# Kernel optimization log

Measured on AMD Instinct MI355X. Metric: run time of the kernel, lower is better.

## Reference

```python
import math
import jax, jax.numpy as jnp
import numpy as np

# ---- hard-coded constants from the source module ----
T_H = 1.5; M = 60; DT = T_H / M; SQDT = math.sqrt(DT)
ALPHA = 0.8; RHO = 0.3; SQ1MR2 = math.sqrt(1.0 - RHO * RHO)
GAMMA = 5.0; KAPPA_Y = 1.2; LB_W = 1e-3
R = 0.02; SIGMA = 0.2; SIGMA_Y = 0.3; THETA_Y = 0.0; PI_CAP = 2.0
RPTS = 128       # sub_batch (one accumulation iteration)
REPEATS = 128    # total repeats == sub_batch -> single loop pass
N_PTS = 32       # number of eval states
HID = 64


def setup_inputs():
    key = jax.random.key(0)
    ks = jax.random.split(key, 8)
    W = 0.8 + 0.4 * jax.random.uniform(ks[0], (N_PTS, 1), jnp.float32)   # W0_range
    Y = -1.0 + 2.0 * jax.random.uniform(ks[1], (N_PTS, 1), jnp.float32)  # Y0_range
    TmT = jnp.full((N_PTS, 1), T_H, jnp.float32)
    B = RPTS * N_PTS
    # [sim(+/-), draw(z1/z2), step, path, 1] -- fresh noise per antithetic branch, as in torch
    noise = jax.random.normal(ks[2], (2, 2, M, B, 1), jnp.float32)
    w1 = 0.1 * jax.random.normal(ks[3], (3, HID), jnp.float32)
    b1 = jnp.zeros((HID,), jnp.float32)
    w2 = 0.1 * jax.random.normal(ks[4], (HID, HID), jnp.float32)
    b2 = jnp.zeros((HID,), jnp.float32)
    w3 = 0.1 * jax.random.normal(ks[5], (HID, 1), jnp.float32)
    b3 = jnp.zeros((1,), jnp.float32)
    return {"W": W, "TmT": TmT, "Y": Y, "noise": noise,
            "w1": w1, "b1": b1, "w2": w2, "b2": b2, "w3": w3, "b3": b3}


def _policy(params, W, TmT, Y):
    w1, b1, w2, b2, w3, b3 = params
    x = jnp.concatenate([W, TmT, Y], axis=-1)          # [B,3]
    h = jnp.tanh(x @ w1 + b1)
    h = jnp.tanh(h @ w2 + b2)
    return h @ w3 + b3                                 # [B,1]


def _simulate(params, W0, Y0, z1, z2, anti):
    """60-step Euler-Maruyama; returns CRRA utility U(W_T), shape [B,1]."""
    logW = jnp.log(jnp.clip(W0, LB_W, None))
    TmT0 = jnp.full_like(W0, T_H)

    def step(carry, zs):
        logW, Y, TmT = carry
        z1s, z2s = zs
        pi = _policy(params, jnp.exp(logW), TmT, Y)
        zW = anti * z1s
        zY = anti * (RHO * z1s + SQ1MR2 * z2s)
        drift = R + pi * (SIGMA * ALPHA * Y)
        var = (pi * SIGMA) ** 2
        logW = logW + (drift - 0.5 * var) * DT + pi * SIGMA * SQDT * zW
        Y = Y + KAPPA_Y * (THETA_Y - Y) * DT + SIGMA_Y * SQDT * zY
        logW = jnp.log(jnp.clip(jnp.exp(logW), LB_W, None))
        return (logW, Y, TmT - DT), None

    (logW, _, _), _ = jax.lax.scan(step, (logW, Y0, TmT0), (z1, z2))
    W_T = jnp.exp(logW)
    return W_T ** (1.0 - GAMMA) / (1.0 - GAMMA)        # gamma != 1


def reference(W, TmT, Y, noise, w1, b1, w2, b2, w3, b3):
    params = (w1, b1, w2, b2, w3, b3)
    n = W.shape[0]
    Wd = jax.lax.stop_gradient(W)   # forward detaches W, Y
    Yd = jax.lax.stop_gradient(Y)
    W0 = jnp.tile(Wd, (RPTS, 1))    # [B,1]
    Y0 = jnp.tile(Yd, (RPTS, 1))
    z1p, z2p = noise[0, 0], noise[0, 1]
    z1m, z2m = noise[1, 0], noise[1, 1]

    def f(W0_, Y0_):
        U = 0.5 * (_simulate(params, W0_, Y0_, z1p, z2p, 1.0)
                   + _simulate(params, W0_, Y0_, z1m, z2m, -1.0))
        # U_avg.sum() as in torch: mean over rpts, sum over eval points
        return jnp.sum(jnp.mean(U.reshape(RPTS, n), axis=0))

    lam_full = jax.grad(f, 0)(W0, Y0)                  # [B,1]

    def g(W0_, Y0_):
        # lam.view(rpts,n,1).mean(0).sum() == sum(lam_full)/rpts
        return jnp.sum(jax.grad(f, 0)(W0_, Y0_)) / RPTS

    dW_full, dY_full = jax.grad(g, (0, 1))(W0, Y0)     # [B,1] each

    inv = 1.0 / REPEATS   # faithful to source accumulation scaling
    lam = lam_full.reshape(RPTS, n, 1).mean(0) * inv
    dlamW = dW_full.reshape(RPTS, n, 1).mean(0) * inv
    dlamY = dY_full.reshape(RPTS, n, 1).mean(0) * inv

    # project_pmp
    mu_minus_r = SIGMA * (ALPHA * Yd)
    coeff = -1.0 / (Wd * dlamW + 1e-8)
    myo = coeff * (lam * (mu_minus_r / SIGMA ** 2))
    hedge = coeff * (SIGMA * RHO * SIGMA_Y * dlamY / SIGMA ** 2)
    return jnp.clip(myo + hedge, -PI_CAP, PI_CAP)      # [n,1]
```

## Files before the change

kernel.cpp:

```cpp
#include <hip/hip_runtime.h>
#include <math.h>

#define HID    64
#define MSTEPS 60
#define NPTS   32
#define RPTSC  128
#define BTOT   (RPTSC*NPTS)
#define NSIM   (2*BTOT)
#define NWAVE  (NSIM/2)
#define NBLK   (NWAVE/4)

#define C_DT     0.025f
#define C_SQDT   0.15811388300841897f
#define C_ALPHA  0.8f
#define C_RHO    0.3f
#define C_SQ1MR2 0.9539392014169456f
#define C_KAPPA  1.2f
#define C_R      0.02f
#define C_SIGMA  0.2f
#define C_SIGY   0.3f
#define C_LBW    1e-3f
#define C_LOGLBW -6.907755279f
#define C_2L2E   2.8853900817779268f

#define WAVE_LDS 3584
#define OFF_DV   2304
#define OFF_DA   3328

typedef _Float16 half8 __attribute__((ext_vector_type(8)));
typedef float    f32x4 __attribute__((ext_vector_type(4)));
typedef _Float16 h2    __attribute__((ext_vector_type(2)));
typedef int      i32x2 __attribute__((ext_vector_type(2)));
typedef int      i32x4 __attribute__((ext_vector_type(4)));

__device__ __forceinline__ float rlanef(float v, int l) {
    return __int_as_float(__builtin_amdgcn_readlane(__float_as_int(v), l));
}
template <int OFF>
__device__ __forceinline__ float swz(float v) {
    return __int_as_float(__builtin_amdgcn_ds_swizzle(__float_as_int(v), OFF));
}
__device__ __forceinline__ f32x4 MFMA(half8 a, half8 b, f32x4 c) {
    return __builtin_amdgcn_mfma_f32_16x16x32_f16(a, b, c, 0, 0, 0);
}
__device__ __forceinline__ int pk16(float a, float b) {
    return __builtin_bit_cast(int, __builtin_amdgcn_cvt_pkrtz(a, b));
}
__device__ __forceinline__ h2 pk2(float a, float b) {
    return __builtin_bit_cast(h2, __builtin_amdgcn_cvt_pkrtz(a, b));
}
__device__ __forceinline__ unsigned permu(unsigned s0, unsigned s1, unsigned sel) {
    return __builtin_amdgcn_perm(s0, s1, sel);
}
__device__ __forceinline__ h2 permh(unsigned s0, unsigned s1, unsigned sel) {
    return __builtin_bit_cast(h2, __builtin_amdgcn_perm(s0, s1, sel));
}
__device__ __forceinline__ float tanh_fast(float xs) {
    return 1.0f - 2.0f * __builtin_amdgcn_rcpf(__builtin_amdgcn_exp2f(xs) + 1.0f);
}
__device__ __forceinline__ i32x2 tr16(unsigned a) {
    i32x2 d;
    asm volatile("ds_read_b64_tr_b16 %0, %1"
                 : "=&v"(d) : "v"(a) : "memory");
    return d;
}
#define LGKM0_FENCE() do { \
    asm volatile("s_waitcnt lgkmcnt(0)" ::: "memory"); \
    __builtin_amdgcn_sched_barrier(0); } while (0)

__global__ __launch_bounds__(256, 4) void sim_kernel(
    const float* __restrict__ noise,
    const float* __restrict__ w1, const float* __restrict__ b1,
    const float* __restrict__ w2, const float* __restrict__ b2,
    const float* __restrict__ w3, const float* __restrict__ b3,
    const float* __restrict__ Wp, const float* __restrict__ Yp,
    float* __restrict__ sd)
{
    __shared__ __align__(16) char smem[4 * WAVE_LDS];
    const int lane = threadIdx.x & 63;
    const int quad = lane >> 4;
    const int mrow = lane & 15;
    const int par  = lane >> 5;
    char* wb = smem + (threadIdx.x >> 6) * WAVE_LDS;

    const int w = __builtin_amdgcn_readfirstlane(
        (int)((blockIdx.x * blockDim.x + threadIdx.x) >> 6));
    const int simb = w >> 11;
    const int pg   = 2*(w & 2047) + par;
    const int i    = pg & (NPTS - 1);

    const float cW  = w1[lane];
    const float cT  = w1[HID + lane];
    const float cYw = w1[2*HID + lane];
    const float b1k = b1[lane];
    const float b2k = b2[lane];
    const float b3v = b3[0];
    const float cW_s  = cW  * C_2L2E;
    const float cT_s  = cT  * C_2L2E;
    const float cYw_s = cYw * C_2L2E;
    const float b1_s  = b1k * C_2L2E;
    const float b2_s  = b2k * C_2L2E;
    const h2 cWh  = pk2(cW, cW);
    const h2 cYwh = pk2(cYw, cYw);
    const h2 cW2m = pk2(-2.0f*cW*cW,  -2.0f*cW*cW);
    const h2 cWYm = pk2(-2.0f*cW*cYw, -2.0f*cW*cYw);
    const h2 hone = {(_Float16)1.0f,  (_Float16)1.0f};
    const h2 m2h  = {(_Float16)-2.0f, (_Float16)-2.0f};

    half8 B00, B01, B02, B03, B10, B11, B12, B13, W30, W31;
    {
        half8 h;
        #define LOADB(dst, q, t) \
            { for (int j = 0; j < 8; ++j) \
                h[j] = (_Float16)w2[((q)*32 + quad*8 + j)*HID + (t)*16 + mrow]; \
              dst = h; }
        LOADB(B00, 0, 0) LOADB(B01, 0, 1) LOADB(B02, 0, 2) LOADB(B03, 0, 3)
        LOADB(B10, 1, 0) LOADB(B11, 1, 1) LOADB(B12, 1, 2) LOADB(B13, 1, 3)
        #undef LOADB
        for (int j = 0; j < 8; ++j) h[j] = (_Float16)w3[0*32 + quad*8 + j];
        W30 = h;
        for (int j = 0; j < 8; ++j) h[j] = (_Float16)w3[1*32 + quad*8 + j];
        W31 = h;
    }
    asm volatile("" : "+v"(B00), "+v"(B01), "+v"(B02), "+v"(B03),
                      "+v"(B10), "+v"(B11), "+v"(B12), "+v"(B13),
                      "+v"(W30), "+v"(W31));

    char* Swp = wb + (lane >> 2) * 144 + (lane & 3) * 32;
    const unsigned wbu  = (unsigned)(size_t)wb;
    const unsigned tA0 = wbu + quad*288 + mrow*2;
    const unsigned tA1 = tA0 + 144;
    const unsigned tB0 = tA0 + 1152;
    const unsigned tB1 = tA0 + 1296;

    const float* zp1 = noise + (size_t)(simb*2 + 0) * MSTEPS * BTOT + pg;
    const float* zp2 = noise + (size_t)(simb*2 + 1) * MSTEPS * BTOT + pg;

    const float anti = simb ? -1.0f : 1.0f;
    const float ksa  = C_SIGMA * C_ALPHA;
    const float ks2  = C_SIGMA * C_SIGMA;
    const float ksn  = anti * C_SIGMA * C_SQDT;
    const float kFy  = ksa * C_DT;
    const float ksd  = ks2 * C_DT;
    const float kv   = 0.5f * ks2 * C_DT;
    const float kRdt = C_R * C_DT;
    const float ky1  = anti * C_SIGY * C_SQDT * C_RHO;
    const float ky2  = anti * C_SIGY * C_SQDT * C_SQ1MR2;
    const float cYfac = 1.0f - C_KAPPA * C_DT;

    const float W0 = Wp[i];
    float L   = __logf(fmaxf(W0, C_LBW));
    float W   = __expf(L);
    float Yv  = Yp[i];
    float tmt = 1.5f;
    float gW  = 1.0f / W0;
    float hWW = -gW * gW;
    float gY  = 0.0f, hWY = 0.0f;
    float cYt = 1.0f;

    #pragma unroll 1
    for (int m = 0; m < MSTEPS; ++m) {
        const float z1 = zp1[(size_t)m * BTOT];
        const float z2 = zp2[(size_t)m * BTOT];

        const float Wb0 = rlanef(W, 0),  Wb1 = rlanef(W, 32);
        const float Yb0 = rlanef(Yv, 0), Yb1 = rlanef(Yv, 32);

        const float base1s = fmaf(tmt, cT_s, b1_s);
        {
            const float t10 = tanh_fast(fmaf(Wb0, cW_s, fmaf(Yb0, cYw_s, base1s)));
            const float t11 = tanh_fast(fmaf(Wb1, cW_s, fmaf(Yb1, cYw_s, base1s)));
            const h2 tp  = pk2(t10, t11);
            const h2 dpp = hone - tp * tp;
            const h2 ddq = tp * dpp;
            const h2 r1 = dpp * cWh;
            const h2 r2 = dpp * cYwh;
            const h2 r3 = ddq * cW2m;
            const h2 r4 = ddq * cWYm;
            const unsigned utp = __builtin_bit_cast(unsigned, tp);
            const unsigned ur1 = __builtin_bit_cast(unsigned, r1);
            const unsigned ur2 = __builtin_bit_cast(unsigned, r2);
            const unsigned ur3 = __builtin_bit_cast(unsigned, r3);
            const unsigned ur4 = __builtin_bit_cast(unsigned, r4);
            i32x4 lo, hi;
            lo[0] = (int)permu(ur1, utp, 0x05040100u);
            lo[1] = (int)permu(ur3, ur2, 0x05040100u);
            lo[2] = (int)(ur4 & 0xFFFFu);
            lo[3] = 0;
            hi[0] = (int)permu(ur1, utp, 0x07060302u);
            hi[1] = (int)permu(ur3, ur2, 0x07060302u);
            hi[2] = (int)(ur4 >> 16);
            hi[3] = 0;
            *(i32x4*)(Swp)      = lo;
            *(i32x4*)(Swp + 16) = hi;
        }

        i32x2 ta0 = tr16(tA0), ta1 = tr16(tA1);
        i32x2 tb0 = tr16(tB0), tb1 = tr16(tB1);
        LGKM0_FENCE();
        i32x4 ia0; ia0[0]=ta0[0]; ia0[1]=ta0[1]; ia0[2]=ta1[0]; ia0[3]=ta1[1];
        i32x4 ia1; ia1[0]=tb0[0]; ia1[1]=tb0[1]; ia1[2]=tb1[0]; ia1[3]=tb1[1];
        half8 af0 = __builtin_bit_cast(half8, ia0);
        half8 af1 = __builtin_bit_cast(half8, ia1);

        f32x4 acc[4];
        const f32x4 zz = {0.f, 0.f, 0.f, 0.f};
        acc[0] = MFMA(af1, B10, MFMA(af0, B00, zz));
        acc[1] = MFMA(af1, B11, MFMA(af0, B01, zz));
        acc[2] = MFMA(af1, B12, MFMA(af0, B02, zz));
        acc[3] = MFMA(af1, B13, MFMA(af0, B03, zz));

        {
            const int p = quad >> 1;
            if (!(quad & 1)) {
                #pragma unroll
                for (int t = 0; t < 4; ++t) {
                    int2 v;
                    v.x = pk16(acc[t].x, acc[t].y);
                    v.y = pk16(acc[t].z, acc[t].w);
                    *(int2*)(wb + OFF_DV + ((t*16 + mrow) << 4) + (p << 3)) = v;
                }
            } else {
                #pragma unroll
                for (int t = 0; t < 4; ++t)
                    *(_Float16*)(wb + OFF_DA + ((t*16 + mrow) << 2) + (p << 1)) =
                        (_Float16)acc[t].x;
            }
        }

        const f32x4 dvv = *(const f32x4*)(wb + OFF_DV + lane*16);
        const h2 awyp   = *(const h2*)(wb + OFF_DA + lane*4);
        {
            const unsigned q0 = __builtin_bit_cast(unsigned, dvv.x);
            const unsigned q1 = __builtin_bit_cast(unsigned, dvv.y);
            const unsigned q2 = __builtin_bit_cast(unsigned, dvv.z);
            const unsigned q3 = __builtin_bit_cast(unsigned, dvv.w);
            const h2 a0p  = permh(q2, q0, 0x05040100);
            const h2 aWp  = permh(q2, q0, 0x07060302);
            const h2 aYp  = permh(q3, q1, 0x05040100);
            const h2 aWWp = permh(q3, q1, 0x07060302);

            const float t20 = tanh_fast(fmaf((float)a0p.x, C_2L2E, b2_s));
            const float t21 = tanh_fast(fmaf((float)a0p.y, C_2L2E, b2_s));
            const h2 t2p = pk2(t20, t21);
            const h2 d2p = hone - t2p * t2p;
            const h2 qp  = (m2h * (t2p * d2p)) * aWp;
            const h2 s1 = d2p * aWp;
            const h2 s2 = d2p * aYp;
            const h2 s3 = qp * aWp + d2p * aWWp;
            const h2 s4 = qp * aYp + d2p * awyp;
            const unsigned ut = __builtin_bit_cast(unsigned, t2p);
            const unsigned u1 = __builtin_bit_cast(unsigned, s1);
            const unsigned u2 = __builtin_bit_cast(unsigned, s2);
            const unsigned u3 = __builtin_bit_cast(unsigned, s3);
            const unsigned u4 = __builtin_bit_cast(unsigned, s4);
            i32x4 lo, hi;
            lo[0] = (int)permu(u1, ut, 0x05040100u);
            lo[1] = (int)permu(u3, u2, 0x05040100u);
            lo[2] = (int)(u4 & 0xFFFFu);
            lo[3] = 0;
            hi[0] = (int)permu(u1, ut, 0x07060302u);
            hi[1] = (int)permu(u3, u2, 0x07060302u);
            hi[2] = (int)(u4 >> 16);
            hi[3] = 0;
            *(i32x4*)(Swp)      = lo;
            *(i32x4*)(Swp + 16) = hi;
        }

        i32x2 tc0 = tr16(tA0), tc1 = tr16(tA1);
        i32x2 td0 = tr16(tB0), td1 = tr16(tB1);
        LGKM0_FENCE();
        i32x4 ib0; ib0[0]=tc0[0]; ib0[1]=tc0[1]; ib0[2]=tc1[0]; ib0[3]=tc1[1];
        i32x4 ib1; ib1[0]=td0[0]; ib1[1]=td0[1]; ib1[2]=td1[0]; ib1[3]=td1[1];
        half8 bf0 = __builtin_bit_cast(half8, ib0);
        half8 bf1 = __builtin_bit_cast(half8, ib1);
        f32x4 acc4 = MFMA(bf1, W31, MFMA(bf0, W30, zz));

        const float pi  = swz<0x0000>(acc4.x) + b3v;
        const float pW  = swz<0x0000>(acc4.y);
        const float pY  = swz<0x0000>(acc4.z);
        const float pWW = swz<0x0000>(acc4.w);
        const float pWY = swz<0x0200>(acc4.x);

        const float Sn    = ksn * z1;
        const float say   = ksa * Yv;
        const float G     = fmaf(-ks2, pi, say);
        const float GdtSn = fmaf(G, C_DT, Sn);

        const float w2v  = W * W;
        const float piL  = pW * W;
        const float piLL = fmaf(pWW, w2v, piL);
        const float piY  = pY;
        const float piLY = pWY * W;

        const float pi2  = pi * pi;
        const float Lnew = fmaf(pi, fmaf(say, C_DT, Sn),
                                fmaf(-kv, pi2, L + kRdt));

        const float F_L  = fmaf(piL, GdtSn, 1.0f);
        const float F_Y  = fmaf(piY, GdtSn, kFy * pi);
        const float piL2 = piL * piL;
        const float F_LL = fmaf(piLL, GdtSn, -(ksd * piL2));
        const float F_LY = fmaf(piLY, GdtSn, piL * fmaf(-ksd, piY, kFy));

        const float gW2  = gW * gW;
        const float hWWn = fmaf(F_LL, gW2, F_L * hWW);
        const float hWYn = fmaf(F_LL, gW * gY,
                                fmaf(F_LY, gW * cYt, F_L * hWY));
        const float gWn  = F_L * gW;
        const float gYn  = fmaf(F_Y, cYt, F_L * gY);

        Yv  = fmaf(ky2, z2, fmaf(ky1, z1, cYfac * Yv));
        cYt *= cYfac;

        const float We   = __expf(Lnew);
        const bool  clip = (We < C_LBW);
        L   = clip ? C_LOGLBW : Lnew;
        W   = clip ? C_LBW    : We;
        gW  = clip ? 0.0f : gWn;
        gY  = clip ? 0.0f : gYn;
        hWW = clip ? 0.0f : hWWn;
        hWY = clip ? 0.0f : hWYn;
        tmt -= C_DT;
    }

    const float E   = __expf(-4.0f * L);
    const float d1  = E * gW;
    const float d2v = fmaf(-4.0f * E, gW * gW, E * hWW);
    const float d3v = fmaf(-4.0f * E, gW * gY, E * hWY);

    if ((lane & 31) == 0) {
        const int branch = simb * BTOT + pg;
        sd[         branch] = 0.5f * d1;
        sd[  NSIM + branch] = 0.5f * d2v;
        sd[2*NSIM + branch] = 0.5f * d3v;
    }
}

__global__ __launch_bounds__(512) void proj_kernel(
    const float* __restrict__ sd,
    const float* __restrict__ Wp,
    const float* __restrict__ Yp,
    float* __restrict__ out)
{
    __shared__ float red[3 * 512];
    const int tid = threadIdx.x;
    const int i = tid & 31;
    const int c = tid >> 5;
    float lam = 0.f, dW = 0.f, dY = 0.f;
    #pragma unroll 4
    for (int jj = 0; jj < 16; ++jj) {
        const int idx = i + ((jj*16 + c) << 5);
        lam += sd[idx];
        dW  += sd[NSIM + idx];
        dY  += sd[2*NSIM + idx];
    }
    red[tid] = lam; red[512 + tid] = dW; red[1024 + tid] = dY;
    __syncthreads();
    if (tid < NPTS) {
        float l = 0.f, w = 0.f, y = 0.f;
        #pragma unroll
        for (int c2 = 0; c2 < 16; ++c2) {
            l += red[c2*32 + i];
            w += red[512 + c2*32 + i];
            y += red[1024 + c2*32 + i];
        }
        l *= (1.0f / 2097152.0f);
        w *= (1.0f / 268435456.0f);
        y *= (1.0f / 268435456.0f);
        const float Wv = Wp[i], Yv = Yp[i];
        const float mmr   = C_SIGMA * (C_ALPHA * Yv);
        const float sig2  = C_SIGMA * C_SIGMA;
        const float coeff = -1.0f / (Wv * w + 1e-8f);
        const float myo   = coeff * (l * (mmr / sig2));
        const float hedge = coeff * (C_SIGMA * C_RHO * C_SIGY * y / sig2);
        float v = myo + hedge;
        v = fminf(fmaxf(v, -2.0f), 2.0f);
        out[i] = v;
    }
}

extern "C" void kernel_launch(void* const* d_in, const int* in_sizes, int n_in,
                              void* d_out, int out_size, void* d_ws, size_t ws_size,
                              hipStream_t stream) {
    const float* Wp    = (const float*)d_in[0];
    const float* Yp    = (const float*)d_in[2];
    const float* noise = (const float*)d_in[3];
    const float* w1    = (const float*)d_in[4];
    const float* b1    = (const float*)d_in[5];
    const float* w2    = (const float*)d_in[6];
    const float* b2    = (const float*)d_in[7];
    const float* w3    = (const float*)d_in[8];
    const float* b3    = (const float*)d_in[9];
    float* out = (float*)d_out;
    float* sd  = (float*)d_ws;

    hipLaunchKernelGGL(sim_kernel, dim3(NBLK), dim3(256), 0, stream,
                       noise, w1, b1, w2, b2, w3, b3, Wp, Yp, sd);
    hipLaunchKernelGGL(proj_kernel, dim3(1), dim3(512), 0, stream, sd, Wp, Yp, out);
}
```

Baseline: 158.1 us.

## Pack three simulation paths per wave instead of two, using fp32 derivative math

Each wave now carries three Monte Carlo paths (lanes 0/21/42) instead of two, which cuts the wave count from 4096 to 2731 single-wave blocks. The MFMA row layout is changed to hold 5 derivative channels for each of 3 paths, and the LDS staging and readback are reworked to match. Packed-half arithmetic is replaced with scalar fp32 math, and the final ds_swizzle broadcasts are replaced with readlanes plus a select. The intent is to cut the total serial MLP work per path. In exchange each wave does more scalar VALU work per step, and launch bounds and occupancy change.

```diff
diff --git a/kernel.cpp b/kernel.cpp
--- a/kernel.cpp
+++ b/kernel.cpp
@@ -7,8 +7,8 @@
 #define RPTSC  128
 #define BTOT   (RPTSC*NPTS)
 #define NSIM   (2*BTOT)
-#define NWAVE  (NSIM/2)
-#define NBLK   (NWAVE/4)
+#define NWAVE3 2731
+#define NBLK3  NWAVE3
 
 #define C_DT     0.025f
 #define C_SQDT   0.15811388300841897f
@@ -23,9 +23,8 @@
 #define C_LOGLBW -6.907755279f
 #define C_2L2E   2.8853900817779268f
 
-#define WAVE_LDS 3584
+#define WAVE_LDS 4352
 #define OFF_DV   2304
-#define OFF_DA   3328
 
 typedef _Float16 half8 __attribute__((ext_vector_type(8)));
 typedef float    f32x4 __attribute__((ext_vector_type(4)));
@@ -36,24 +35,11 @@
 __device__ __forceinline__ float rlanef(float v, int l) {
     return __int_as_float(__builtin_amdgcn_readlane(__float_as_int(v), l));
 }
-template <int OFF>
-__device__ __forceinline__ float swz(float v) {
-    return __int_as_float(__builtin_amdgcn_ds_swizzle(__float_as_int(v), OFF));
-}
 __device__ __forceinline__ f32x4 MFMA(half8 a, half8 b, f32x4 c) {
     return __builtin_amdgcn_mfma_f32_16x16x32_f16(a, b, c, 0, 0, 0);
 }
 __device__ __forceinline__ int pk16(float a, float b) {
     return __builtin_bit_cast(int, __builtin_amdgcn_cvt_pkrtz(a, b));
-}
-__device__ __forceinline__ h2 pk2(float a, float b) {
-    return __builtin_bit_cast(h2, __builtin_amdgcn_cvt_pkrtz(a, b));
-}
-__device__ __forceinline__ unsigned permu(unsigned s0, unsigned s1, unsigned sel) {
-    return __builtin_amdgcn_perm(s0, s1, sel);
-}
-__device__ __forceinline__ h2 permh(unsigned s0, unsigned s1, unsigned sel) {
-    return __builtin_bit_cast(h2, __builtin_amdgcn_perm(s0, s1, sel));
 }
 __device__ __forceinline__ float tanh_fast(float xs) {
     return 1.0f - 2.0f * __builtin_amdgcn_rcpf(__builtin_amdgcn_exp2f(xs) + 1.0f);
@@ -68,7 +54,14 @@
     asm volatile("s_waitcnt lgkmcnt(0)" ::: "memory"); \
     __builtin_amdgcn_sched_barrier(0); } while (0)
 
-__global__ __launch_bounds__(256, 4) void sim_kernel(
+__device__ __forceinline__ float f16lo(int d) {
+    return (float)__builtin_bit_cast(h2, d).x;
+}
+__device__ __forceinline__ float f16hi(int d) {
+    return (float)__builtin_bit_cast(h2, d).y;
+}
+
+__global__ __launch_bounds__(64, 3) void sim_kernel(
     const float* __restrict__ noise,
     const float* __restrict__ w1, const float* __restrict__ b1,
     const float* __restrict__ w2, const float* __restrict__ b2,
@@ -76,17 +69,19 @@
     const float* __restrict__ Wp, const float* __restrict__ Yp,
     float* __restrict__ sd)
 {
-    __shared__ __align__(16) char smem[4 * WAVE_LDS];
+    __shared__ __align__(16) char smem[WAVE_LDS];
     const int lane = threadIdx.x & 63;
     const int quad = lane >> 4;
     const int mrow = lane & 15;
-    const int par  = lane >> 5;
-    char* wb = smem + (threadIdx.x >> 6) * WAVE_LDS;
-
-    const int w = __builtin_amdgcn_readfirstlane(
-        (int)((blockIdx.x * blockDim.x + threadIdx.x) >> 6));
-    const int simb = w >> 11;
-    const int pg   = 2*(w & 2047) + par;
+    char* wb = smem;
+
+    const int w = blockIdx.x;
+    const int t3 = (lane >= 21) + (lane >= 42);
+    const int b  = 3*w + t3;
+    const bool valid = (b < NSIM);
+    const int bc   = valid ? b : (NSIM - 1);
+    const int simb = bc >> 12;
+    const int pg   = bc & (BTOT - 1);
     const int i    = pg & (NPTS - 1);
 
     const float cW  = w1[lane];
@@ -100,12 +95,8 @@
     const float cYw_s = cYw * C_2L2E;
     const float b1_s  = b1k * C_2L2E;
     const float b2_s  = b2k * C_2L2E;
-    const h2 cWh  = pk2(cW, cW);
-    const h2 cYwh = pk2(cYw, cYw);
-    const h2 cW2m = pk2(-2.0f*cW*cW,  -2.0f*cW*cW);
-    const h2 cWYm = pk2(-2.0f*cW*cYw, -2.0f*cW*cYw);
-    const h2 hone = {(_Float16)1.0f,  (_Float16)1.0f};
-    const h2 m2h  = {(_Float16)-2.0f, (_Float16)-2.0f};
+    const float m2cW2 = -2.0f * cW * cW;
+    const float m2cWY = -2.0f * cW * cYw;
 
     half8 B00, B01, B02, B03, B10, B11, B12, B13, W30, W31;
     {
@@ -127,11 +118,13 @@
                       "+v"(W30), "+v"(W31));
 
     char* Swp = wb + (lane >> 2) * 144 + (lane & 3) * 32;
-    const unsigned wbu  = (unsigned)(size_t)wb;
+    const unsigned wbu = (unsigned)(size_t)wb;
     const unsigned tA0 = wbu + quad*288 + mrow*2;
     const unsigned tA1 = tA0 + 144;
     const unsigned tB0 = tA0 + 1152;
     const unsigned tB1 = tA0 + 1296;
+    char* dvw = wb + OFF_DV + mrow*32 + quad*8;
+    char* dvr = wb + OFF_DV + lane*32;
 
     const float* zp1 = noise + (size_t)(simb*2 + 0) * MSTEPS * BTOT + pg;
     const float* zp2 = noise + (size_t)(simb*2 + 1) * MSTEPS * BTOT + pg;
@@ -163,34 +156,26 @@
         const float z1 = zp1[(size_t)m * BTOT];
         const float z2 = zp2[(size_t)m * BTOT];
 
-        const float Wb0 = rlanef(W, 0),  Wb1 = rlanef(W, 32);
-        const float Yb0 = rlanef(Yv, 0), Yb1 = rlanef(Yv, 32);
+        const float Wb0 = rlanef(W, 0), Wb1 = rlanef(W, 21), Wb2 = rlanef(W, 42);
+        const float Yb0 = rlanef(Yv, 0), Yb1 = rlanef(Yv, 21), Yb2 = rlanef(Yv, 42);
 
         const float base1s = fmaf(tmt, cT_s, b1_s);
         {
-            const float t10 = tanh_fast(fmaf(Wb0, cW_s, fmaf(Yb0, cYw_s, base1s)));
-            const float t11 = tanh_fast(fmaf(Wb1, cW_s, fmaf(Yb1, cYw_s, base1s)));
-            const h2 tp  = pk2(t10, t11);
-            const h2 dpp = hone - tp * tp;
-            const h2 ddq = tp * dpp;
-            const h2 r1 = dpp * cWh;
-            const h2 r2 = dpp * cYwh;
-            const h2 r3 = ddq * cW2m;
-            const h2 r4 = ddq * cWYm;
-            const unsigned utp = __builtin_bit_cast(unsigned, tp);
-            const unsigned ur1 = __builtin_bit_cast(unsigned, r1);
-            const unsigned ur2 = __builtin_bit_cast(unsigned, r2);
-            const unsigned ur3 = __builtin_bit_cast(unsigned, r3);
-            const unsigned ur4 = __builtin_bit_cast(unsigned, r4);
+            const float t1a = tanh_fast(fmaf(Wb0, cW_s, fmaf(Yb0, cYw_s, base1s)));
+            const float t1b = tanh_fast(fmaf(Wb1, cW_s, fmaf(Yb1, cYw_s, base1s)));
+            const float t1c = tanh_fast(fmaf(Wb2, cW_s, fmaf(Yb2, cYw_s, base1s)));
+            const float dpa = fmaf(-t1a, t1a, 1.0f), tda = t1a * dpa;
+            const float dpb = fmaf(-t1b, t1b, 1.0f), tdb = t1b * dpb;
+            const float dpc = fmaf(-t1c, t1c, 1.0f), tdc = t1c * dpc;
             i32x4 lo, hi;
-            lo[0] = (int)permu(ur1, utp, 0x05040100u);
-            lo[1] = (int)permu(ur3, ur2, 0x05040100u);
-            lo[2] = (int)(ur4 & 0xFFFFu);
-            lo[3] = 0;
-            hi[0] = (int)permu(ur1, utp, 0x07060302u);
-            hi[1] = (int)permu(ur3, ur2, 0x07060302u);
-            hi[2] = (int)(ur4 >> 16);
-            hi[3] = 0;
+            lo[0] = pk16(t1a,        dpa * cW);
+            lo[1] = pk16(dpa * cYw,  tda * m2cW2);
+            lo[2] = pk16(tda * m2cWY, t1b);
+            lo[3] = pk16(dpb * cW,   dpb * cYw);
+            hi[0] = pk16(tdb * m2cW2, tdb * m2cWY);
+            hi[1] = pk16(t1c,        dpc * cW);
+            hi[2] = pk16(dpc * cYw,  tdc * m2cW2);
+            hi[3] = pk16(tdc * m2cWY, 0.0f);
             *(i32x4*)(Swp)      = lo;
             *(i32x4*)(Swp + 16) = hi;
         }
@@ -210,59 +195,51 @@
         acc[2] = MFMA(af1, B12, MFMA(af0, B02, zz));
         acc[3] = MFMA(af1, B13, MFMA(af0, B03, zz));
 
+        #pragma unroll
+        for (int t = 0; t < 4; ++t) {
+            i32x2 v;
+            v[0] = pk16(acc[t].x, acc[t].y);
+            v[1] = pk16(acc[t].z, acc[t].w);
+            *(i32x2*)(dvw + t*512) = v;
+        }
+
+        const i32x4 D0 = *(const i32x4*)(dvr);
+        const i32x4 D1 = *(const i32x4*)(dvr + 16);
         {
-            const int p = quad >> 1;
-            if (!(quad & 1)) {
-                #pragma unroll
-                for (int t = 0; t < 4; ++t) {
-                    int2 v;
-                    v.x = pk16(acc[t].x, acc[t].y);
-                    v.y = pk16(acc[t].z, acc[t].w);
-                    *(int2*)(wb + OFF_DV + ((t*16 + mrow) << 4) + (p << 3)) = v;
-                }
-            } else {
-                #pragma unroll
-                for (int t = 0; t < 4; ++t)
-                    *(_Float16*)(wb + OFF_DA + ((t*16 + mrow) << 2) + (p << 1)) =
-                        (_Float16)acc[t].x;
-            }
-        }
-
-        const f32x4 dvv = *(const f32x4*)(wb + OFF_DV + lane*16);
-        const h2 awyp   = *(const h2*)(wb + OFF_DA + lane*4);
-        {
-            const unsigned q0 = __builtin_bit_cast(unsigned, dvv.x);
-            const unsigned q1 = __builtin_bit_cast(unsigned, dvv.y);
-            const unsigned q2 = __builtin_bit_cast(unsigned, dvv.z);
-            const unsigned q3 = __builtin_bit_cast(unsigned, dvv.w);
-            const h2 a0p  = permh(q2, q0, 0x05040100);
-            const h2 aWp  = permh(q2, q0, 0x07060302);
-            const h2 aYp  = permh(q3, q1, 0x05040100);
-            const h2 aWWp = permh(q3, q1, 0x07060302);
-
-            const float t20 = tanh_fast(fmaf((float)a0p.x, C_2L2E, b2_s));
-            const float t21 = tanh_fast(fmaf((float)a0p.y, C_2L2E, b2_s));
-            const h2 t2p = pk2(t20, t21);
-            const h2 d2p = hone - t2p * t2p;
-            const h2 qp  = (m2h * (t2p * d2p)) * aWp;
-            const h2 s1 = d2p * aWp;
-            const h2 s2 = d2p * aYp;
-            const h2 s3 = qp * aWp + d2p * aWWp;
-            const h2 s4 = qp * aYp + d2p * awyp;
-            const unsigned ut = __builtin_bit_cast(unsigned, t2p);
-            const unsigned u1 = __builtin_bit_cast(unsigned, s1);
-            const unsigned u2 = __builtin_bit_cast(unsigned, s2);
-            const unsigned u3 = __builtin_bit_cast(unsigned, s3);
-            const unsigned u4 = __builtin_bit_cast(unsigned, s4);
+            const float a0a = f16lo(D0[0]), aWa = f16hi(D0[0]);
+            const float aYa = f16lo(D0[1]), aWWa = f16hi(D0[1]);
+            const float awya = f16lo(D0[2]);
+            const float a0b = f16hi(D0[2]), aWb = f16lo(D0[3]);
+            const float aYb = f16hi(D0[3]), aWWb = f16lo(D1[0]);
+            const float awyb = f16hi(D1[0]);
+            const float a0c = f16lo(D1[1]), aWc = f16hi(D1[1]);
+            const float aYc = f16lo(D1[2]), aWWc = f16hi(D1[2]);
+            const float awyc = f16lo(D1[3]);
+
+            const float t2a = tanh_fast(fmaf(a0a, C_2L2E, b2_s));
+            const float t2b = tanh_fast(fmaf(a0b, C_2L2E, b2_s));
+            const float t2c = tanh_fast(fmaf(a0c, C_2L2E, b2_s));
+            const float d2a = fmaf(-t2a, t2a, 1.0f), qa = -2.0f*(t2a*d2a)*aWa;
+            const float d2b = fmaf(-t2b, t2b, 1.0f), qb = -2.0f*(t2b*d2b)*aWb;
+            const float d2c = fmaf(-t2c, t2c, 1.0f), qc = -2.0f*(t2c*d2c)*aWc;
+            const float s1a = d2a*aWa, s2a = d2a*aYa;
+            const float s3a = fmaf(qa, aWa, d2a*aWWa);
+            const float s4a = fmaf(qa, aYa, d2a*awya);
+            const float s1b = d2b*aWb, s2b = d2b*aYb;
+            const float s3b = fmaf(qb, aWb, d2b*aWWb);
+            const float s4b = fmaf(qb, aYb, d2b*awyb);
+            const float s1c = d2c*aWc, s2c = d2c*aYc;
+            const float s3c = fmaf(qc, aWc, d2c*aWWc);
+            const float s4c = fmaf(qc, aYc, d2c*awyc);
             i32x4 lo, hi;
-            lo[0] = (int)permu(u1, ut, 0x05040100u);
-            lo[1] = (int)permu(u3, u2, 0x05040100u);
-            lo[2] = (int)(u4 & 0xFFFFu);
-            lo[3] = 0;
-            hi[0] = (int)permu(u1, ut, 0x07060302u);
-            hi[1] = (int)permu(u3, u2, 0x07060302u);
-            hi[2] = (int)(u4 >> 16);
-            hi[3] = 0;
+            lo[0] = pk16(t2a, s1a);
+            lo[1] = pk16(s2a, s3a);
+            lo[2] = pk16(s4a, t2b);
+            lo[3] = pk16(s1b, s2b);
+            hi[0] = pk16(s3b, s4b);
+            hi[1] = pk16(t2c, s1c);
+            hi[2] = pk16(s2c, s3c);
+            hi[3] = pk16(s4c, 0.0f);
             *(i32x4*)(Swp)      = lo;
             *(i32x4*)(Swp + 16) = hi;
         }
@@ -276,11 +253,19 @@
         half8 bf1 = __builtin_bit_cast(half8, ib1);
         f32x4 acc4 = MFMA(bf1, W31, MFMA(bf0, W30, zz));
 
-        const float pi  = swz<0x0000>(acc4.x) + b3v;
-        const float pW  = swz<0x0000>(acc4.y);
-        const float pY  = swz<0x0000>(acc4.z);
-        const float pWW = swz<0x0000>(acc4.w);
-        const float pWY = swz<0x0200>(acc4.x);
+        const float v0  = rlanef(acc4.x,  0), v1  = rlanef(acc4.y,  0);
+        const float v2  = rlanef(acc4.z,  0), v3  = rlanef(acc4.w,  0);
+        const float v4  = rlanef(acc4.x, 16), v5  = rlanef(acc4.y, 16);
+        const float v6  = rlanef(acc4.z, 16), v7  = rlanef(acc4.w, 16);
+        const float v8  = rlanef(acc4.x, 32), v9  = rlanef(acc4.y, 32);
+        const float v10 = rlanef(acc4.z, 32), v11 = rlanef(acc4.w, 32);
+        const float v12 = rlanef(acc4.x, 48), v13 = rlanef(acc4.y, 48);
+        const float v14 = rlanef(acc4.z, 48);
+        const float pi  = (t3 == 0 ? v0 : t3 == 1 ? v5  : v10) + b3v;
+        const float pW  =  t3 == 0 ? v1 : t3 == 1 ? v6  : v11;
+        const float pY  =  t3 == 0 ? v2 : t3 == 1 ? v7  : v12;
+        const float pWW =  t3 == 0 ? v3 : t3 == 1 ? v8  : v13;
+        const float pWY =  t3 == 0 ? v4 : t3 == 1 ? v9  : v14;
 
         const float Sn    = ksn * z1;
         const float say   = ksa * Yv;
@@ -329,11 +314,10 @@
     const float d2v = fmaf(-4.0f * E, gW * gW, E * hWW);
     const float d3v = fmaf(-4.0f * E, gW * gY, E * hWY);
 
-    if ((lane & 31) == 0) {
-        const int branch = simb * BTOT + pg;
-        sd[         branch] = 0.5f * d1;
-        sd[  NSIM + branch] = 0.5f * d2v;
-        sd[2*NSIM + branch] = 0.5f * d3v;
+    if (valid && (lane == 0 || lane == 21 || lane == 42)) {
+        sd[         b] = 0.5f * d1;
+        sd[  NSIM + b] = 0.5f * d2v;
+        sd[2*NSIM + b] = 0.5f * d3v;
     }
 }
 
@@ -395,7 +379,7 @@
     float* out = (float*)d_out;
     float* sd  = (float*)d_ws;
 
-    hipLaunchKernelGGL(sim_kernel, dim3(NBLK), dim3(256), 0, stream,
+    hipLaunchKernelGGL(sim_kernel, dim3(NBLK3), dim3(64), 0, stream,
                        noise, w1, b1, w2, b2, w3, b3, Wp, Yp, sd);
     hipLaunchKernelGGL(proj_kernel, dim3(1), dim3(512), 0, stream, sd, Wp, Yp, out);
 }
```

Measured after the change: 163.3 us. 3.3% more time.
